# Kernel tuning notes

Measured on AMD Instinct MI355X. Metric: run time of the kernel, lower is better.

## Reference

```python
import jax, jax.numpy as jnp
import numpy as np

ROTARY = 32
MAX_POS = 10000

# Precompute complex rotary table exactly as the module does: rows are positions
# 0..9999 and the slice used is freqs_cis[-S:] (positions MAX_POS-S .. MAX_POS-1).
_ang = np.outer(np.arange(MAX_POS), 1.0 / 10000.0 ** (np.arange(0, ROTARY, 2) / ROTARY))
FREQS_CIS = jnp.asarray(np.cos(_ang) + 1j * np.sin(_ang), dtype=jnp.complex64)  # [MAX_POS, ROTARY//2]


def _apply_rotary(x):
    # x: [B, S, H, ROTARY]; split-half -> complex, multiply, interleave back.
    B, S, H, R = x.shape
    z = x.astype(jnp.float32).reshape(B, S, H, 2, R // 2)
    zc = jax.lax.complex(z[..., 0, :], z[..., 1, :])            # [B,S,H,R//2]
    zc = zc * FREQS_CIS[None, MAX_POS - S:, None, :]
    out = jnp.stack((jnp.real(zc), jnp.imag(zc)), axis=-1)       # [B,S,H,R//2,2] (interleaved)
    return out.reshape(B, S, H, R).astype(x.dtype)


def setup_inputs() -> dict:
    key = jax.random.key(0)
    ks = jax.random.split(key, 10)
    B, S, D, H, HD = 4, 1024, 4096, 32, 128
    scale = 0.02
    return {
        "x": jax.random.normal(ks[0], (B, S, D), dtype=jnp.float32),
        "attn_bias": jax.random.normal(ks[1], (1, 1, S, S), dtype=jnp.float32),
        "wq_kernel": jax.random.normal(ks[2], (D, H, HD), dtype=jnp.float32) * scale,
        "wq_bias": jax.random.normal(ks[3], (H, HD), dtype=jnp.float32) * scale,
        "wk_kernel": jax.random.normal(ks[4], (D, H, HD), dtype=jnp.float32) * scale,
        "wk_bias": jax.random.normal(ks[5], (H, HD), dtype=jnp.float32) * scale,
        "wv_kernel": jax.random.normal(ks[6], (D, H, HD), dtype=jnp.float32) * scale,
        "wv_bias": jax.random.normal(ks[7], (H, HD), dtype=jnp.float32) * scale,
        "wo_kernel": jax.random.normal(ks[8], (H, HD, D), dtype=jnp.float32) * scale,
        "wo_bias": jax.random.normal(ks[9], (D,), dtype=jnp.float32) * scale,
    }


def reference(x, attn_bias, wq_kernel, wq_bias, wk_kernel, wk_bias,
              wv_kernel, wv_bias, wo_kernel, wo_bias):
    # Projections (DenseGeneral -> [B, S, H, HD])
    q = jnp.einsum('bsd,dhk->bshk', x, wq_kernel) + wq_bias
    k = jnp.einsum('bsd,dhk->bshk', x, wk_kernel) + wk_bias
    v = jnp.einsum('bsd,dhk->bshk', x, wv_kernel) + wv_bias
    # Empty-cache prefill: update_cache just stores k/v unchanged.
    # Partial rotary on the first ROTARY channels.
    q = jnp.concatenate((_apply_rotary(q[..., :ROTARY]), q[..., ROTARY:]), axis=3)
    k = jnp.concatenate((_apply_rotary(k[..., :ROTARY]), k[..., ROTARY:]), axis=3)
    head_dim = k.shape[3]
    p = jnp.einsum('bqhd,bkhd->bhqk', q, k) / head_dim ** 0.5
    attn = jax.nn.softmax(p + attn_bias, axis=3)
    o = jnp.einsum('bhqk,bkhd->bqhd', attn, v)
    return jnp.einsum('bqhd,hdm->bqm', o, wo_kernel) + wo_bias
```

## Files before the change

kernel.cpp:

```cpp
#include <hip/hip_runtime.h>
#include <hip/hip_bf16.h>

typedef unsigned short u16;
typedef __attribute__((ext_vector_type(8))) short bf16x8;
typedef __attribute__((ext_vector_type(4))) float f32x4;

#define MFMA16(a, b, c) __builtin_amdgcn_mfma_f32_16x16x32_bf16((a), (b), (c), 0, 0, 0)

#define GLD16(src, dst)                                                        \
    __builtin_amdgcn_global_load_lds(                                          \
        (const __attribute__((address_space(1))) void*)(src),                  \
        (__attribute__((address_space(3))) void*)(dst), 16, 0, 0)

__device__ __forceinline__ float bf2f(u16 u) {
    union { unsigned int i; float f; } v;
    v.i = ((unsigned int)u) << 16;
    return v.f;
}
__device__ __forceinline__ u16 f2bf(float f) {
    unsigned int x = __float_as_uint(f);
    x += 0x7FFFu + ((x >> 16) & 1u);
    return (u16)(x >> 16);
}

__global__ void rope_table_kernel(float2* __restrict__ tab) {
    int i = blockIdx.x * 256 + threadIdx.x;
    if (i >= 1024 * 16) return;
    int s = i >> 4, p = i & 15;
    double ang = (double)(8976 + s) * pow(10000.0, -(double)p / 16.0);
    tab[i] = make_float2((float)cos(ang), (float)sin(ang));
}

__global__ __launch_bounds__(256) void xcast_kernel(const float* __restrict__ X,
                                                    u16* __restrict__ Xb, int n) {
    int i = (blockIdx.x * 256 + threadIdx.x) * 8;
    if (i >= n) return;
    float4 f0 = *(const float4*)(X + i);
    float4 f1 = *(const float4*)(X + i + 4);
    union { u16 u[8]; uint4 v; } o;
    o.u[0] = f2bf(f0.x); o.u[1] = f2bf(f0.y); o.u[2] = f2bf(f0.z); o.u[3] = f2bf(f0.w);
    o.u[4] = f2bf(f1.x); o.u[5] = f2bf(f1.y); o.u[6] = f2bf(f1.z); o.u[7] = f2bf(f1.w);
    *(uint4*)(Xb + i) = o.v;
}

__global__ __launch_bounds__(256) void wt_kernel(const float* __restrict__ W,
                                                 u16* __restrict__ WT, int K, int N) {
    __shared__ u16 t[64][72];
    const int kt = blockIdx.y * 64, nt = blockIdx.x * 64;
    const int tid = threadIdx.x;
#pragma unroll
    for (int i = 0; i < 4; i++) {
        int cid = tid + i * 256;
        int k = cid >> 4, c = cid & 15;
        float4 f = *(const float4*)(W + (size_t)(kt + k) * N + nt + c * 4);
        t[c * 4 + 0][k] = f2bf(f.x);
        t[c * 4 + 1][k] = f2bf(f.y);
        t[c * 4 + 2][k] = f2bf(f.z);
        t[c * 4 + 3][k] = f2bf(f.w);
    }
    __syncthreads();
#pragma unroll
    for (int i = 0; i < 2; i++) {
        int cid = tid + i * 256;
        int n = cid >> 3, c = cid & 7;
        union { u16 u[8]; uint4 v; } o;
#pragma unroll
        for (int j = 0; j < 8; j++) o.u[j] = t[n][c * 8 + j];
        *(uint4*)(WT + (size_t)(nt + n) * K + kt + c * 8) = o.v;
    }
}

__global__ void rope_apply_kernel(u16* __restrict__ q, u16* __restrict__ k,
                                  const float2* __restrict__ tab) {
    int i = blockIdx.x * 256 + threadIdx.x;
    if (i >= 4 * 1024 * 32) return;
    int s = (i >> 5) & 1023;
    const float2* tp = tab + s * 16;
    u16* ptrs[2] = { q + (size_t)i * 128, k + (size_t)i * 128 };
#pragma unroll
    for (int t = 0; t < 2; t++) {
        u16* p = ptrs[t];
        u16 buf[32], outb[32];
        *(uint4*)(buf)      = *(const uint4*)(p);
        *(uint4*)(buf + 8)  = *(const uint4*)(p + 8);
        *(uint4*)(buf + 16) = *(const uint4*)(p + 16);
        *(uint4*)(buf + 24) = *(const uint4*)(p + 24);
#pragma unroll
        for (int j = 0; j < 16; j++) {
            float a = bf2f(buf[j]), b = bf2f(buf[j + 16]);
            float c = tp[j].x, sn = tp[j].y;
            outb[2 * j]     = f2bf(a * c - b * sn);
            outb[2 * j + 1] = f2bf(a * sn + b * c);
        }
        *(uint4*)(p)      = *(uint4*)(outb);
        *(uint4*)(p + 8)  = *(uint4*)(outb + 8);
        *(uint4*)(p + 16) = *(uint4*)(outb + 16);
        *(uint4*)(p + 24) = *(uint4*)(outb + 24);
    }
}

template<int OUT_F32>
__global__ __launch_bounds__(256) void gemm_bt_kernel(
    const u16* __restrict__ A, const u16* __restrict__ BT,
    const float* __restrict__ bias, void* __restrict__ Cv,
    int M, int N, int K) {
    constexpr int BK = 32;
    __shared__ u16 As[128 * BK];
    __shared__ u16 Bs[128 * BK];

    const int tid  = threadIdx.x;
    const int lane = tid & 63;
    const int wave = tid >> 6;
    const int quad = lane >> 4;
    const int lm   = lane & 15;
    const int m0 = blockIdx.y * 128;
    const int n0 = blockIdx.x * 128;
    const int wm = (wave >> 1) * 64;
    const int wn = (wave & 1) * 64;

    const f32x4 fz = {0.f, 0.f, 0.f, 0.f};
    f32x4 acc[4][4];
#pragma unroll
    for (int i = 0; i < 4; i++)
#pragma unroll
        for (int j = 0; j < 4; j++) acc[i][j] = fz;

    const int g0 = wave * 64 + lane;
    const int g1 = g0 + 256;
    const u16* aS0 = A  + (size_t)(m0 + (g0 >> 2)) * K + (g0 & 3) * 8;
    const u16* aS1 = A  + (size_t)(m0 + (g1 >> 2)) * K + (g1 & 3) * 8;
    const u16* bS0 = BT + (size_t)(n0 + (g0 >> 2)) * K + (g0 & 3) * 8;
    const u16* bS1 = BT + (size_t)(n0 + (g1 >> 2)) * K + (g1 & 3) * 8;
    u16* aD0 = As + (size_t)wave * 512;
    u16* aD1 = aD0 + 2048;
    u16* bD0 = Bs + (size_t)wave * 512;
    u16* bD1 = bD0 + 2048;

    for (int k0 = 0; k0 < K; k0 += BK) {
        GLD16(aS0 + k0, aD0);
        GLD16(aS1 + k0, aD1);
        GLD16(bS0 + k0, bD0);
        GLD16(bS1 + k0, bD1);
        __syncthreads();

        bf16x8 a[4], b[4];
#pragma unroll
        for (int i = 0; i < 4; i++)
            a[i] = *(const bf16x8*)(As + (wm + i * 16 + lm) * BK + quad * 8);
#pragma unroll
        for (int i = 0; i < 4; i++)
            b[i] = *(const bf16x8*)(Bs + (wn + i * 16 + lm) * BK + quad * 8);
#pragma unroll
        for (int i = 0; i < 4; i++)
#pragma unroll
            for (int j = 0; j < 4; j++)
                acc[i][j] = MFMA16(a[i], b[j], acc[i][j]);
        __syncthreads();
    }

#pragma unroll
    for (int j = 0; j < 4; j++) {
        int col = n0 + wn + j * 16 + lm;
        float bv = bias[col];
#pragma unroll
        for (int i = 0; i < 4; i++) {
            int rowb = m0 + wm + i * 16 + quad * 4;
#pragma unroll
            for (int r = 0; r < 4; r++) {
                float v = acc[i][j][r] + bv;
                if (OUT_F32) ((float*)Cv)[(size_t)(rowb + r) * N + col] = v;
                else         ((u16*)Cv)[(size_t)(rowb + r) * N + col] = f2bf(v);
            }
        }
    }
}

__global__ __launch_bounds__(256) void attn_kernel(
    const u16* __restrict__ Q, const u16* __restrict__ Kv,
    const u16* __restrict__ V, const float* __restrict__ Bias,
    u16* __restrict__ O) {
    constexpr int S = 1024, H = 32, HD = 128;
    constexpr int KST = 136;
    constexpr int VST = 40;
    __shared__ u16 Ks[32 * KST];
    __shared__ u16 Vst[128 * VST];
    __shared__ u16 Ps[4 * 16 * VST];

    const int tid  = threadIdx.x;
    const int lane = tid & 63;
    const int wave = tid >> 6;
    const int quad = lane >> 4;
    const int lm   = lane & 15;
    const int qt = blockIdx.x;
    const int h  = blockIdx.y;
    const int b  = blockIdx.z;
    const int qrow = qt * 64 + wave * 16;

    const u16* qb = Q + (((size_t)b * S + qrow + lm) * H + h) * HD;
    bf16x8 qf[4];
#pragma unroll
    for (int f = 0; f < 4; f++)
        qf[f] = *(const bf16x8*)(qb + f * 32 + quad * 8);

    float m_run[4], l_run[4], alpha[4];
#pragma unroll
    for (int r = 0; r < 4; r++) { m_run[r] = -3.0e38f; l_run[r] = 0.f; }
    const f32x4 fz = {0.f, 0.f, 0.f, 0.f};
    f32x4 oacc[8];
#pragma unroll
    for (int t = 0; t < 8; t++) oacc[t] = fz;

    const float scale = 0.08838834764831845f;

    for (int kt = 0; kt < S / 32; kt++) {
        const int key0 = kt * 32;
#pragma unroll
        for (int i = 0; i < 2; i++) {
            int c = tid + i * 256;
            int row = c >> 4, part = c & 15;
            const uint4* src = (const uint4*)(Kv + (((size_t)b * S + key0 + row) * H + h) * HD + part * 8);
            *(uint4*)(Ks + row * KST + part * 8) = *src;
        }
#pragma unroll
        for (int i = 0; i < 2; i++) {
            int w = tid + i * 256;
            int hd = w & 127, kc = w >> 7;
            const u16* src = V + (((size_t)b * S + key0 + kc * 8) * H + h) * HD + hd;
            union { u16 u[8]; uint4 v; } t;
#pragma unroll
            for (int j = 0; j < 8; j++) t.u[j] = src[(size_t)j * H * HD];
            *(uint4*)(Vst + hd * VST + kc * 8) = t.v;
        }
        __syncthreads();

        f32x4 sc[2];
#pragma unroll
        for (int kt2 = 0; kt2 < 2; kt2++) {
            f32x4 c = fz;
#pragma unroll
            for (int f = 0; f < 4; f++) {
                bf16x8 kf = *(const bf16x8*)(Ks + (kt2 * 16 + lm) * KST + f * 32 + quad * 8);
                c = MFMA16(qf[f], kf, c);
            }
            sc[kt2] = c;
        }

#pragma unroll
        for (int r = 0; r < 4; r++) {
            int qr = qrow + quad * 4 + r;
            float s0 = sc[0][r] * scale + Bias[(size_t)qr * S + key0 + lm];
            float s1 = sc[1][r] * scale + Bias[(size_t)qr * S + key0 + 16 + lm];
            float mx = fmaxf(s0, s1);
#pragma unroll
            for (int d = 1; d < 16; d <<= 1) mx = fmaxf(mx, __shfl_xor(mx, d));
            float mnew = fmaxf(m_run[r], mx);
            alpha[r] = __expf(m_run[r] - mnew);
            float p0 = __expf(s0 - mnew);
            float p1 = __expf(s1 - mnew);
            float ps = p0 + p1;
#pragma unroll
            for (int d = 1; d < 16; d <<= 1) ps += __shfl_xor(ps, d);
            l_run[r] = l_run[r] * alpha[r] + ps;
            m_run[r] = mnew;
            Ps[wave * (16 * VST) + (quad * 4 + r) * VST + lm]      = f2bf(p0);
            Ps[wave * (16 * VST) + (quad * 4 + r) * VST + 16 + lm] = f2bf(p1);
        }
#pragma unroll
        for (int t = 0; t < 8; t++)
#pragma unroll
            for (int r = 0; r < 4; r++) oacc[t][r] *= alpha[r];
        __syncthreads();

        bf16x8 pf = *(const bf16x8*)(Ps + wave * (16 * VST) + lm * VST + quad * 8);
#pragma unroll
        for (int t = 0; t < 8; t++) {
            bf16x8 vf = *(const bf16x8*)(Vst + (t * 16 + lm) * VST + quad * 8);
            oacc[t] = MFMA16(pf, vf, oacc[t]);
        }
        __syncthreads();
    }

    u16* ob = O + (((size_t)b * S + qrow) * H + h) * HD;
#pragma unroll
    for (int r = 0; r < 4; r++) {
        float inv = 1.0f / l_run[r];
#pragma unroll
        for (int t = 0; t < 8; t++) {
            int hd = t * 16 + lm;
            ob[(size_t)(quad * 4 + r) * H * HD + hd] = f2bf(oacc[t][r] * inv);
        }
    }
}

extern "C" void kernel_launch(void* const* d_in, const int* in_sizes, int n_in,
                              void* d_out, int out_size, void* d_ws, size_t ws_size,
                              hipStream_t stream) {
    const float* x   = (const float*)d_in[0];
    const float* ab  = (const float*)d_in[1];
    const float* wq  = (const float*)d_in[2];
    const float* wqb = (const float*)d_in[3];
    const float* wk  = (const float*)d_in[4];
    const float* wkb = (const float*)d_in[5];
    const float* wv  = (const float*)d_in[6];
    const float* wvb = (const float*)d_in[7];
    const float* wo  = (const float*)d_in[8];
    const float* wob = (const float*)d_in[9];
    float* out = (float*)d_out;

    const size_t MAT = (size_t)4096 * 4096;
    u16* qb = (u16*)d_ws;
    u16* kb = qb + MAT;
    u16* vb = kb + MAT;
    u16* ob = vb + MAT;
    u16* xb = ob + MAT;
    u16* wt = xb + MAT;
    float2* tab = (float2*)(wt + MAT);

    rope_table_kernel<<<64, 256, 0, stream>>>(tab);
    xcast_kernel<<<8192, 256, 0, stream>>>(x, xb, (int)MAT);

    dim3 g(32, 32);
    dim3 wtg(64, 64);
    wt_kernel<<<wtg, 256, 0, stream>>>(wq, wt, 4096, 4096);
    gemm_bt_kernel<0><<<g, 256, 0, stream>>>(xb, wt, wqb, qb, 4096, 4096, 4096);
    wt_kernel<<<wtg, 256, 0, stream>>>(wk, wt, 4096, 4096);
    gemm_bt_kernel<0><<<g, 256, 0, stream>>>(xb, wt, wkb, kb, 4096, 4096, 4096);
    wt_kernel<<<wtg, 256, 0, stream>>>(wv, wt, 4096, 4096);
    gemm_bt_kernel<0><<<g, 256, 0, stream>>>(xb, wt, wvb, vb, 4096, 4096, 4096);

    rope_apply_kernel<<<512, 256, 0, stream>>>(qb, kb, tab);
    attn_kernel<<<dim3(16, 32, 4), 256, 0, stream>>>(qb, kb, vb, ab, ob);

    wt_kernel<<<wtg, 256, 0, stream>>>(wo, wt, 4096, 4096);
    gemm_bt_kernel<1><<<g, 256, 0, stream>>>(ob, wt, wob, out, 4096, 4096, 4096);
}
```

Measured before the change: 1.376 ms.

## Pre-transpose V and load K/V tiles via direct-to-LDS with XOR swizzle

Adds a separate kernel that transposes V into a per-head [HD, S] layout, replacing the strided 2-byte gathers that previously built the transposed V tile inside the attention loop. The attention kernel now uses 64-key tiles loaded with global_load_lds (16B per lane) into unpadded shared buffers with an XOR swizzle to avoid bank conflicts. It also skips the O rescale when the running max does not change and raises wave priority around the MFMA blocks. The costs are an extra transpose pass over V, a reused workspace buffer (xb) to hold it, and larger shared-memory tiles.

```diff
diff --git a/kernel.cpp b/kernel.cpp
--- a/kernel.cpp
+++ b/kernel.cpp
@@ -70,6 +70,34 @@
     }
 }
 
+__global__ __launch_bounds__(256) void vtrans_kernel(const u16* __restrict__ V,
+                                                     u16* __restrict__ VT) {
+    __shared__ u16 t[64][74];
+    const int tid = threadIdx.x;
+    const int bh = blockIdx.z;
+    const int b = bh >> 5, h = bh & 31;
+    const int s0 = blockIdx.x * 64, d0 = blockIdx.y * 64;
+#pragma unroll
+    for (int i = 0; i < 2; i++) {
+        int c = tid + i * 256;
+        int sr = c >> 3, dp = c & 7;
+        union { u16 u[8]; uint4 v; } in;
+        in.v = *(const uint4*)(V + (((size_t)b * 1024 + s0 + sr) * 32 + h) * 128 + d0 + dp * 8);
+#pragma unroll
+        for (int j = 0; j < 8; j++) t[dp * 8 + j][sr] = in.u[j];
+    }
+    __syncthreads();
+#pragma unroll
+    for (int i = 0; i < 2; i++) {
+        int c = tid + i * 256;
+        int dr = c >> 3, sp = c & 7;
+        union { u16 u[8]; uint4 v; } o;
+#pragma unroll
+        for (int j = 0; j < 8; j++) o.u[j] = t[dr][sp * 8 + j];
+        *(uint4*)(VT + (((size_t)b * 32 + h) * 128 + d0 + dr) * 1024 + s0 + sp * 8) = o.v;
+    }
+}
+
 __global__ void rope_apply_kernel(u16* __restrict__ q, u16* __restrict__ k,
                                   const float2* __restrict__ tab) {
     int i = blockIdx.x * 256 + threadIdx.x;
@@ -177,14 +205,13 @@
 
 __global__ __launch_bounds__(256) void attn_kernel(
     const u16* __restrict__ Q, const u16* __restrict__ Kv,
-    const u16* __restrict__ V, const float* __restrict__ Bias,
+    const u16* __restrict__ VT, const float* __restrict__ Bias,
     u16* __restrict__ O) {
     constexpr int S = 1024, H = 32, HD = 128;
-    constexpr int KST = 136;
-    constexpr int VST = 40;
-    __shared__ u16 Ks[32 * KST];
-    __shared__ u16 Vst[128 * VST];
-    __shared__ u16 Ps[4 * 16 * VST];
+    constexpr int PST = 72;
+    __shared__ u16 Ks[64 * 128];
+    __shared__ u16 Vst[128 * 64];
+    __shared__ u16 Ps[4 * 16 * PST];
 
     const int tid  = threadIdx.x;
     const int lane = tid & 63;
@@ -202,6 +229,21 @@
     for (int f = 0; f < 4; f++)
         qf[f] = *(const bf16x8*)(qb + f * 32 + quad * 8);
 
+    const u16* kSrc[4];
+    const u16* vSrc[4];
+    u16* kDst[4];
+    u16* vDst[4];
+#pragma unroll
+    for (int i = 0; i < 4; i++) {
+        int g = i * 256 + wave * 64 + lane;
+        int krow = g >> 4, kpart = (g & 15) ^ (krow & 7);
+        kSrc[i] = Kv + (((size_t)b * S + krow) * H + h) * HD + kpart * 8;
+        kDst[i] = Ks + (size_t)(i * 256 + wave * 64) * 8;
+        int vrow = g >> 3, vpart = (g & 7) ^ (vrow & 7);
+        vSrc[i] = VT + (((size_t)b * H + h) * HD + vrow) * S + vpart * 8;
+        vDst[i] = Vst + (size_t)(i * 256 + wave * 64) * 8;
+    }
+
     float m_run[4], l_run[4], alpha[4];
 #pragma unroll
     for (int r = 0; r < 4; r++) { m_run[r] = -3.0e38f; l_run[r] = 0.f; }
@@ -211,72 +253,83 @@
     for (int t = 0; t < 8; t++) oacc[t] = fz;
 
     const float scale = 0.08838834764831845f;
-
-    for (int kt = 0; kt < S / 32; kt++) {
-        const int key0 = kt * 32;
-#pragma unroll
-        for (int i = 0; i < 2; i++) {
-            int c = tid + i * 256;
-            int row = c >> 4, part = c & 15;
-            const uint4* src = (const uint4*)(Kv + (((size_t)b * S + key0 + row) * H + h) * HD + part * 8);
-            *(uint4*)(Ks + row * KST + part * 8) = *src;
-        }
-#pragma unroll
-        for (int i = 0; i < 2; i++) {
-            int w = tid + i * 256;
-            int hd = w & 127, kc = w >> 7;
-            const u16* src = V + (((size_t)b * S + key0 + kc * 8) * H + h) * HD + hd;
-            union { u16 u[8]; uint4 v; } t;
-#pragma unroll
-            for (int j = 0; j < 8; j++) t.u[j] = src[(size_t)j * H * HD];
-            *(uint4*)(Vst + hd * VST + kc * 8) = t.v;
-        }
-        __syncthreads();
-
-        f32x4 sc[2];
-#pragma unroll
-        for (int kt2 = 0; kt2 < 2; kt2++) {
+    const int lx = lm & 7;
+
+    for (int kt = 0; kt < S / 64; kt++) {
+        const int key0 = kt * 64;
+        const size_t kOff = (size_t)key0 * H * HD;
+#pragma unroll
+        for (int i = 0; i < 4; i++) GLD16(kSrc[i] + kOff, kDst[i]);
+#pragma unroll
+        for (int i = 0; i < 4; i++) GLD16(vSrc[i] + key0, vDst[i]);
+        __syncthreads();
+
+        f32x4 sc[4];
+        __builtin_amdgcn_s_setprio(1);
+#pragma unroll
+        for (int kt2 = 0; kt2 < 4; kt2++) {
             f32x4 c = fz;
 #pragma unroll
             for (int f = 0; f < 4; f++) {
-                bf16x8 kf = *(const bf16x8*)(Ks + (kt2 * 16 + lm) * KST + f * 32 + quad * 8);
+                bf16x8 kf = *(const bf16x8*)(Ks + (kt2 * 16 + lm) * 128 + ((4 * f + quad) ^ lx) * 8);
                 c = MFMA16(qf[f], kf, c);
             }
             sc[kt2] = c;
         }
-
+        __builtin_amdgcn_s_setprio(0);
+
+        bool need = false;
 #pragma unroll
         for (int r = 0; r < 4; r++) {
             int qr = qrow + quad * 4 + r;
-            float s0 = sc[0][r] * scale + Bias[(size_t)qr * S + key0 + lm];
-            float s1 = sc[1][r] * scale + Bias[(size_t)qr * S + key0 + 16 + lm];
-            float mx = fmaxf(s0, s1);
+            const float* bp = Bias + (size_t)qr * S + key0 + lm;
+            float s0 = sc[0][r] * scale + bp[0];
+            float s1 = sc[1][r] * scale + bp[16];
+            float s2 = sc[2][r] * scale + bp[32];
+            float s3 = sc[3][r] * scale + bp[48];
+            float mx = fmaxf(fmaxf(s0, s1), fmaxf(s2, s3));
 #pragma unroll
             for (int d = 1; d < 16; d <<= 1) mx = fmaxf(mx, __shfl_xor(mx, d));
-            float mnew = fmaxf(m_run[r], mx);
-            alpha[r] = __expf(m_run[r] - mnew);
-            float p0 = __expf(s0 - mnew);
-            float p1 = __expf(s1 - mnew);
-            float ps = p0 + p1;
+            if (mx > m_run[r]) {
+                alpha[r] = __expf(m_run[r] - mx);
+                m_run[r] = mx;
+                need = true;
+            } else {
+                alpha[r] = 1.f;
+            }
+            float p0 = __expf(s0 - m_run[r]);
+            float p1 = __expf(s1 - m_run[r]);
+            float p2 = __expf(s2 - m_run[r]);
+            float p3 = __expf(s3 - m_run[r]);
+            float ps = (p0 + p1) + (p2 + p3);
 #pragma unroll
             for (int d = 1; d < 16; d <<= 1) ps += __shfl_xor(ps, d);
             l_run[r] = l_run[r] * alpha[r] + ps;
-            m_run[r] = mnew;
-            Ps[wave * (16 * VST) + (quad * 4 + r) * VST + lm]      = f2bf(p0);
-            Ps[wave * (16 * VST) + (quad * 4 + r) * VST + 16 + lm] = f2bf(p1);
-        }
-#pragma unroll
-        for (int t = 0; t < 8; t++)
-#pragma unroll
-            for (int r = 0; r < 4; r++) oacc[t][r] *= alpha[r];
-        __syncthreads();
-
-        bf16x8 pf = *(const bf16x8*)(Ps + wave * (16 * VST) + lm * VST + quad * 8);
+            u16* pr = Ps + wave * (16 * PST) + (quad * 4 + r) * PST + lm;
+            pr[0]  = f2bf(p0);
+            pr[16] = f2bf(p1);
+            pr[32] = f2bf(p2);
+            pr[48] = f2bf(p3);
+        }
+        if (need) {
+#pragma unroll
+            for (int t = 0; t < 8; t++)
+#pragma unroll
+                for (int r = 0; r < 4; r++) oacc[t][r] *= alpha[r];
+        }
+        __syncthreads();
+
+        bf16x8 pf0 = *(const bf16x8*)(Ps + wave * (16 * PST) + lm * PST + quad * 8);
+        bf16x8 pf1 = *(const bf16x8*)(Ps + wave * (16 * PST) + lm * PST + 32 + quad * 8);
+        __builtin_amdgcn_s_setprio(1);
 #pragma unroll
         for (int t = 0; t < 8; t++) {
-            bf16x8 vf = *(const bf16x8*)(Vst + (t * 16 + lm) * VST + quad * 8);
-            oacc[t] = MFMA16(pf, vf, oacc[t]);
-        }
+            bf16x8 vf0 = *(const bf16x8*)(Vst + (t * 16 + lm) * 64 + (quad ^ lx) * 8);
+            bf16x8 vf1 = *(const bf16x8*)(Vst + (t * 16 + lm) * 64 + ((4 + quad) ^ lx) * 8);
+            oacc[t] = MFMA16(pf0, vf0, oacc[t]);
+            oacc[t] = MFMA16(pf1, vf1, oacc[t]);
+        }
+        __builtin_amdgcn_s_setprio(0);
         __syncthreads();
     }
 
@@ -315,6 +368,7 @@
     u16* xb = ob + MAT;
     u16* wt = xb + MAT;
     float2* tab = (float2*)(wt + MAT);
+    u16* vt = xb;
 
     rope_table_kernel<<<64, 256, 0, stream>>>(tab);
     xcast_kernel<<<8192, 256, 0, stream>>>(x, xb, (int)MAT);
@@ -329,7 +383,8 @@
     gemm_bt_kernel<0><<<g, 256, 0, stream>>>(xb, wt, wvb, vb, 4096, 4096, 4096);
 
     rope_apply_kernel<<<512, 256, 0, stream>>>(qb, kb, tab);
-    attn_kernel<<<dim3(16, 32, 4), 256, 0, stream>>>(qb, kb, vb, ab, ob);
+    vtrans_kernel<<<dim3(16, 2, 128), 256, 0, stream>>>(vb, vt);
+    attn_kernel<<<dim3(16, 32, 4), 256, 0, stream>>>(qb, kb, vt, ab, ob);
 
     wt_kernel<<<wtg, 256, 0, stream>>>(wo, wt, 4096, 4096);
     gemm_bt_kernel<1><<<g, 256, 0, stream>>>(ob, wt, wob, out, 4096, 4096, 4096);
```

Measured after the change: 1.395 ms. About the same (+1.4%).
